# Kernel tuning notes

Hardware: AMD Instinct MI355X
Metric: run time of the kernel (lower is better)

## Reference

```python
import jax, jax.numpy as jnp
import numpy as np

N_EMBD = 768
N_HEAD = 12
NEG = -1e9  # finite stand-in for -inf in the causal part of the FIRE mask


def setup_inputs() -> dict:
    key = jax.random.key(0)
    ks = jax.random.split(key, 6)
    B, T, C = 4, 2048, N_EMBD
    x = jax.random.normal(ks[0], (B, T, C), jnp.float32)
    # FIRE-style per-head additive relative-position bias, masked causally
    bias = jax.random.normal(ks[1], (1, N_HEAD, T, T), jnp.float32)
    causal = jnp.tril(jnp.ones((T, T), bool))
    fire_causal_mask = jnp.where(causal, bias, NEG)
    W_attn = jax.random.normal(ks[2], (C, 3 * C), jnp.float32) * (1.0 / np.sqrt(C))
    b_attn = jax.random.normal(ks[3], (3 * C,), jnp.float32) * 0.02
    W_proj = jax.random.normal(ks[4], (C, C), jnp.float32) * (1.0 / np.sqrt(C))
    b_proj = jax.random.normal(ks[5], (C,), jnp.float32) * 0.02
    return {"x": x, "fire_causal_mask": fire_causal_mask, "W_attn": W_attn,
            "b_attn": b_attn, "W_proj": W_proj, "b_proj": b_proj}


def reference(x, fire_causal_mask, W_attn, b_attn, W_proj, b_proj):
    B, T, C = x.shape
    hd = C // N_HEAD
    qkv = x @ W_attn + b_attn                       # [B, T, 3C]
    q, k, v = jnp.split(qkv, 3, axis=-1)

    def to_heads(t):  # [B, T, C] -> [B, H, T, hd]
        return t.reshape(B, T, N_HEAD, hd).transpose(0, 2, 1, 3)

    q, k, v = to_heads(q), to_heads(k), to_heads(v)
    scale = 1.0 / np.sqrt(hd)
    # SDPA with additive float attn_mask: softmax(q k^T / sqrt(d) + mask) v
    scores = jnp.einsum('bhqd,bhkd->bhqk', q, k) * scale + fire_causal_mask
    p = jax.nn.softmax(scores, axis=-1)
    y = jnp.einsum('bhqk,bhkd->bhqd', p, v)         # [B, H, T, hd]
    y = y.transpose(0, 2, 1, 3).reshape(B, T, C)
    return y @ W_proj + b_proj
```

## Files before the change

### kernel.cpp

```cpp
#include <hip/hip_runtime.h>
#include <hip/hip_bf16.h>
#include <stdint.h>

#define N_HEADC 12
#define T_SEQ   2048
#define C_EMBD  768
#define HD      64

typedef short s16x8 __attribute__((ext_vector_type(8)));
typedef float f32x4 __attribute__((ext_vector_type(4)));
typedef unsigned short u16;
typedef unsigned int   u32;
typedef unsigned long long u64;

__device__ __forceinline__ u16 f2bf(float f) {
  u32 u = __builtin_bit_cast(u32, f);
  u32 r = (u + 0x7FFFu + ((u >> 16) & 1u)) >> 16;
  return (u16)r;
}

__device__ __forceinline__ void async16(const void* g, void* l) {
  u64 ga = (u64)g;
  u32 la = (u32)(u64)l;
  __builtin_amdgcn_global_load_lds(
      (const __attribute__((address_space(1))) u32*)ga,
      (__attribute__((address_space(3))) u32*)la, 16, 0, 0);
}


__global__ __launch_bounds__(256) void k_prep(
    const float4* __restrict__ x4, ushort4* __restrict__ xb4,
    const float* __restrict__ Wa, u16* __restrict__ wat,
    const float* __restrict__ Wp, u16* __restrict__ wpt) {
  __shared__ float tl[64 * 65];
  int bx = blockIdx.x;
  int tid = threadIdx.x;
  if (bx < 6144) {
    int i = bx * 256 + tid;
    float4 v = x4[i];
    ushort4 o;
    o.x = f2bf(v.x); o.y = f2bf(v.y); o.z = f2bf(v.z); o.w = f2bf(v.w);
    xb4[i] = o;
    return;
  }
  const float* in; u16* out; int Kdim, Ndim, n0, k0;
  if (bx < 6144 + 432) {
    int idx = bx - 6144;
    in = Wa; out = wat; Kdim = C_EMBD; Ndim = 3 * C_EMBD;
    n0 = (idx % 36) * 64; k0 = (idx / 36) * 64;
  } else {
    int idx = bx - 6576;
    in = Wp; out = wpt; Kdim = C_EMBD; Ndim = C_EMBD;
    n0 = (idx % 12) * 64; k0 = (idx / 12) * 64;
  }
  int r0 = tid >> 4;
  int cb = (tid & 15) * 4;
#pragma unroll
  for (int g = 0; g < 4; ++g) {
    int r = r0 + g * 16;
    float4 v = *(const float4*)&in[(size_t)(k0 + r) * Ndim + n0 + cb];
    tl[r * 65 + cb + 0] = v.x;
    tl[r * 65 + cb + 1] = v.y;
    tl[r * 65 + cb + 2] = v.z;
    tl[r * 65 + cb + 3] = v.w;
  }
  __syncthreads();
  int rr0 = tid >> 3;
  int cc = (tid & 7) * 8;
#pragma unroll
  for (int g = 0; g < 2; ++g) {
    int rr = rr0 + g * 32;
    u16 tmp[8];
#pragma unroll
    for (int j = 0; j < 8; ++j) tmp[j] = f2bf(tl[(cc + j) * 65 + rr]);
    *(uint4*)&out[(size_t)(n0 + rr) * Kdim + k0 + cc] = *(uint4*)tmp;
  }
}

__global__ __launch_bounds__(256) void k_transpose_v(const u16* __restrict__ v,
                                                     u16* __restrict__ vt) {
  __shared__ u16 tl[64 * 65];
  int t0 = blockIdx.x * 64;
  int bh = blockIdx.y;
  int tid = threadIdx.x;
  const u16* vb = v + (size_t)bh * T_SEQ * HD;
  u16* vtb = vt + (size_t)bh * HD * T_SEQ;
#pragma unroll
  for (int g = 0; g < 2; ++g) {
    int id = g * 256 + tid;
    int r = id >> 3, c = id & 7;
    uint4 raw = *(const uint4*)&vb[(size_t)(t0 + r) * HD + c * 8];
    u16 tmp[8];
    *(uint4*)tmp = raw;
#pragma unroll
    for (int j = 0; j < 8; ++j) tl[r * 65 + c * 8 + j] = tmp[j];
  }
  __syncthreads();
#pragma unroll
  for (int g = 0; g < 2; ++g) {
    int id = g * 256 + tid;
    int d = id >> 3, cw = id & 7;
    u16 tmp[8];
#pragma unroll
    for (int j = 0; j < 8; ++j) tmp[j] = tl[(cw * 8 + j) * 65 + d];
    *(uint4*)&vtb[(size_t)d * T_SEQ + t0 + cw * 8] = *(uint4*)tmp;
  }
}


#define GEMM_BODY(K)                                                          \
  __shared__ __align__(16) u16 Al[128 * 64];                                  \
  __shared__ __align__(16) u16 Bl[128 * 64];                                  \
  int n0 = blockIdx.x * 128, m0 = blockIdx.y * 128;                           \
  int tid = threadIdx.x, lane = tid & 63;                                     \
  int w = tid >> 6, quad = lane >> 4, l16 = lane & 15;                        \
  int wm = (w >> 1) * 64, wn = (w & 1) * 64;                                  \
  f32x4 acc[4][4];                                                            \
  _Pragma("unroll") for (int a = 0; a < 4; ++a)                               \
      _Pragma("unroll") for (int b = 0; b < 4; ++b)                           \
          acc[a][b] = (f32x4){0.f, 0.f, 0.f, 0.f};                            \
  for (int kt = 0; kt < (K); kt += 64) {                                      \
    __syncthreads();                                                          \
    _Pragma("unroll") for (int g = 0; g < 4; ++g) {                           \
      int id = g * 256 + tid;                                                 \
      int r = id >> 3, c = id & 7, cs = c ^ (r & 7);                          \
      async16(A + (size_t)(m0 + r) * (K) + kt + cs * 8, (char*)Al + id * 16); \
      async16(Bt + (size_t)(n0 + r) * (K) + kt + cs * 8, (char*)Bl + id * 16);\
    }                                                                         \
    __syncthreads();                                                          \
    _Pragma("unroll") for (int s = 0; s < 2; ++s) {                           \
      s16x8 af[4], bfr[4];                                                    \
      _Pragma("unroll") for (int mi = 0; mi < 4; ++mi) {                      \
        int m = wm + mi * 16 + l16;                                           \
        af[mi] = *(const s16x8*)&Al[m * 64 + (((s * 4 + quad) ^ (m & 7)) * 8)];\
      }                                                                       \
      _Pragma("unroll") for (int ni = 0; ni < 4; ++ni) {                      \
        int n = wn + ni * 16 + l16;                                           \
        bfr[ni] = *(const s16x8*)&Bl[n * 64 + (((s * 4 + quad) ^ (n & 7)) * 8)];\
      }                                                                       \
      _Pragma("unroll") for (int mi = 0; mi < 4; ++mi)                        \
          _Pragma("unroll") for (int ni = 0; ni < 4; ++ni)                    \
              acc[mi][ni] = __builtin_amdgcn_mfma_f32_16x16x32_bf16(          \
                  af[mi], bfr[ni], acc[mi][ni], 0, 0, 0);                     \
    }                                                                         \
  }

__global__ __launch_bounds__(256) void k_gemm_qkv(
    const u16* __restrict__ A, const u16* __restrict__ Bt,
    const float* __restrict__ bias, u16* __restrict__ qh,
    u16* __restrict__ kh, u16* __restrict__ vh) {
  GEMM_BODY(C_EMBD)
#pragma unroll
  for (int ni = 0; ni < 4; ++ni) {
    int n = n0 + wn + ni * 16 + l16;
    float bv = bias[n];
    int part = n / C_EMBD;
    int nn = n - part * C_EMBD;
    int hh = nn >> 6, d = nn & 63;
    u16* dst = part == 0 ? qh : (part == 1 ? kh : vh);
#pragma unroll
    for (int mi = 0; mi < 4; ++mi) {
      int mbase = m0 + wm + mi * 16 + quad * 4;
#pragma unroll
      for (int r = 0; r < 4; ++r) {
        int m = mbase + r;
        int b = m >> 11, t = m & 2047;
        dst[((size_t)(b * N_HEADC + hh) * T_SEQ + t) * HD + d] =
            f2bf(acc[mi][ni][r] + bv);
      }
    }
  }
}


__global__ __launch_bounds__(256) void k_gemm_out(
    const u16* __restrict__ A, const u16* __restrict__ Bt,
    const float* __restrict__ bias, float* __restrict__ out) {
  __shared__ __align__(16) u16 Al[128 * 64];
  __shared__ __align__(16) u16 Bl[64 * 64];
  int n0 = blockIdx.x * 64, m0 = blockIdx.y * 128;
  int tid = threadIdx.x, lane = tid & 63;
  int w = tid >> 6, quad = lane >> 4, l16 = lane & 15;
  int wm = (w >> 1) * 64, wn = (w & 1) * 32;
  f32x4 acc[4][2];
#pragma unroll
  for (int a = 0; a < 4; ++a)
#pragma unroll
    for (int b = 0; b < 2; ++b) acc[a][b] = (f32x4){0.f, 0.f, 0.f, 0.f};
  for (int kt = 0; kt < C_EMBD; kt += 64) {
    __syncthreads();
#pragma unroll
    for (int g = 0; g < 4; ++g) {
      int id = g * 256 + tid;
      int r = id >> 3, c = id & 7, cs = c ^ (r & 7);
      async16(A + (size_t)(m0 + r) * C_EMBD + kt + cs * 8, (char*)Al + id * 16);
    }
#pragma unroll
    for (int g = 0; g < 2; ++g) {
      int id = g * 256 + tid;
      int r = id >> 3, c = id & 7, cs = c ^ (r & 7);
      async16(Bt + (size_t)(n0 + r) * C_EMBD + kt + cs * 8, (char*)Bl + id * 16);
    }
    __syncthreads();
#pragma unroll
    for (int s = 0; s < 2; ++s) {
      s16x8 af[4], bfr[2];
#pragma unroll
      for (int mi = 0; mi < 4; ++mi) {
        int m = wm + mi * 16 + l16;
        af[mi] = *(const s16x8*)&Al[m * 64 + (((s * 4 + quad) ^ (m & 7)) * 8)];
      }
#pragma unroll
      for (int ni = 0; ni < 2; ++ni) {
        int n = wn + ni * 16 + l16;
        bfr[ni] = *(const s16x8*)&Bl[n * 64 + (((s * 4 + quad) ^ (n & 7)) * 8)];
      }
#pragma unroll
      for (int mi = 0; mi < 4; ++mi)
#pragma unroll
        for (int ni = 0; ni < 2; ++ni)
          acc[mi][ni] = __builtin_amdgcn_mfma_f32_16x16x32_bf16(
              af[mi], bfr[ni], acc[mi][ni], 0, 0, 0);
    }
  }
#pragma unroll
  for (int ni = 0; ni < 2; ++ni) {
    int n = n0 + wn + ni * 16 + l16;
    float bv = bias[n];
#pragma unroll
    for (int mi = 0; mi < 4; ++mi) {
      int mbase = m0 + wm + mi * 16 + quad * 4;
#pragma unroll
      for (int r = 0; r < 4; ++r)
        out[(size_t)(mbase + r) * C_EMBD + n] = acc[mi][ni][r] + bv;
    }
  }
}


__global__ __launch_bounds__(256, 4) void k_attn(
    const u16* __restrict__ qh, const u16* __restrict__ kh,
    const u16* __restrict__ vth, const float* __restrict__ mask,
    u16* __restrict__ y) {
  __shared__ __align__(16) u16 Kl[2][64 * 64];
  __shared__ __align__(16) u16 Vl[2][64 * 64];
  __shared__ __align__(16) u16 Pl[4][16 * 64];
  int bx0 = blockIdx.x;
  int by = blockIdx.y;
  int h = by >> 2, b = by & 3;
  int bh = b * N_HEADC + h;
  int tid = threadIdx.x, lane = tid & 63;
  int w = tid >> 6, quad = lane >> 4, l16 = lane & 15;

  const u16* kg = kh + (size_t)bh * T_SEQ * HD;
  const u16* vg = vth + (size_t)bh * HD * T_SEQ;

  int r_st = tid >> 3, c_st = tid & 7, cs_st = c_st ^ (r_st & 7);
  int r_st2 = r_st + 32, cs_st2 = c_st ^ (r_st2 & 7);
  int id0 = tid * 16, id1 = (256 + tid) * 16;

#pragma unroll 1
  for (int ph = 0; ph < 2; ++ph) {
    int bx = ph == 0 ? (31 - bx0) : bx0;
    int qw = bx * 64 + w * 16;

    const u16* qg = qh + ((size_t)bh * T_SEQ + qw + l16) * HD;
    s16x8 qf0 = *(const s16x8*)(qg + quad * 8);
    s16x8 qf1 = *(const s16x8*)(qg + 32 + quad * 8);
    const float* mg = mask + ((size_t)h * T_SEQ + qw + quad * 4) * T_SEQ + l16;

    f32x4 yacc[4];
#pragma unroll
    for (int i = 0; i < 4; ++i) yacc[i] = (f32x4){0.f, 0.f, 0.f, 0.f};
    float lsum[4] = {0.f, 0.f, 0.f, 0.f};

    int nkt = bx + 1;
    if (ph) __syncthreads();
    async16(kg + (size_t)r_st * HD + cs_st * 8, (char*)Kl[0] + id0);
    async16(vg + (size_t)r_st * T_SEQ + cs_st * 8, (char*)Vl[0] + id0);
    async16(kg + (size_t)r_st2 * HD + cs_st2 * 8, (char*)Kl[0] + id1);
    async16(vg + (size_t)r_st2 * T_SEQ + cs_st2 * 8, (char*)Vl[0] + id1);

    float mcur[16];
#pragma unroll
    for (int r = 0; r < 4; ++r)
#pragma unroll
      for (int nt = 0; nt < 4; ++nt)
        mcur[r * 4 + nt] = mg[(size_t)r * T_SEQ + nt * 16];

    for (int kt = 0; kt < nkt; ++kt) {
      int cur = kt & 1;
      __syncthreads();
      if (kt + 1 < nkt) {
        int nb = (kt + 1) * 64;
        async16(kg + (size_t)(nb + r_st) * HD + cs_st * 8, (char*)Kl[1 - cur] + id0);
        async16(vg + (size_t)r_st * T_SEQ + nb + cs_st * 8, (char*)Vl[1 - cur] + id0);
        async16(kg + (size_t)(nb + r_st2) * HD + cs_st2 * 8, (char*)Kl[1 - cur] + id1);
        async16(vg + (size_t)r_st2 * T_SEQ + nb + cs_st2 * 8, (char*)Vl[1 - cur] + id1);
      }
      int nb_m = (kt + 1 < nkt ? kt + 1 : kt) * 64;
      float mnxt[16];
#pragma unroll
      for (int r = 0; r < 4; ++r)
#pragma unroll
        for (int nt = 0; nt < 4; ++nt)
          mnxt[r * 4 + nt] = mg[(size_t)r * T_SEQ + nb_m + nt * 16];

      f32x4 sacc[4];
#pragma unroll
      for (int nt = 0; nt < 4; ++nt) sacc[nt] = (f32x4){0.f, 0.f, 0.f, 0.f};
#pragma unroll
      for (int nt = 0; nt < 4; ++nt) {
        int row = nt * 16 + l16;
        s16x8 kf0 = *(const s16x8*)&Kl[cur][row * 64 + ((quad ^ (row & 7)) * 8)];
        sacc[nt] = __builtin_amdgcn_mfma_f32_16x16x32_bf16(qf0, kf0, sacc[nt], 0, 0, 0);
        s16x8 kf1 = *(const s16x8*)&Kl[cur][row * 64 + (((4 + quad) ^ (row & 7)) * 8)];
        sacc[nt] = __builtin_amdgcn_mfma_f32_16x16x32_bf16(qf1, kf1, sacc[nt], 0, 0, 0);
      }

      u16* pw = &Pl[w][0];
#pragma unroll
      for (int r = 0; r < 4; ++r) {
        int prow = quad * 4 + r;
#pragma unroll
        for (int nt = 0; nt < 4; ++nt) {
          float val = __expf(fmaf(sacc[nt][r], 0.125f, mcur[r * 4 + nt]));
          lsum[r] += val;
          u32 u = __builtin_bit_cast(u32, val);
          int chunk = (nt * 2 + (l16 >> 3)) ^ (prow & 7);
          pw[prow * 64 + chunk * 8 + (l16 & 7)] = (u16)((u + 0x8000u) >> 16);
        }
      }

#pragma unroll
      for (int s = 0; s < 2; ++s) {
        s16x8 pf = *(const s16x8*)&Pl[w][l16 * 64 + (((s * 4 + quad) ^ (l16 & 7)) * 8)];
#pragma unroll
        for (int nt = 0; nt < 4; ++nt) {
          int row = nt * 16 + l16;
          s16x8 vf = *(const s16x8*)&Vl[cur][row * 64 + (((s * 4 + quad) ^ (row & 7)) * 8)];
          yacc[nt] = __builtin_amdgcn_mfma_f32_16x16x32_bf16(pf, vf, yacc[nt], 0, 0, 0);
        }
      }

#pragma unroll
      for (int i = 0; i < 16; ++i) mcur[i] = mnxt[i];
    }

    u16* yb = y + ((size_t)b * T_SEQ + qw + quad * 4) * C_EMBD + h * HD + l16;
#pragma unroll
    for (int r = 0; r < 4; ++r) {
      float l = lsum[r];
      l += __shfl_xor(l, 1);
      l += __shfl_xor(l, 2);
      l += __shfl_xor(l, 4);
      l += __shfl_xor(l, 8);
      float inv = 1.0f / l;
#pragma unroll
      for (int nt = 0; nt < 4; ++nt)
        yb[(size_t)r * C_EMBD + nt * 16] = f2bf(yacc[nt][r] * inv);
    }
  }
}


extern "C" void kernel_launch(void* const* d_in, const int* in_sizes, int n_in,
                              void* d_out, int out_size, void* d_ws, size_t ws_size,
                              hipStream_t stream) {
  (void)in_sizes; (void)n_in; (void)out_size; (void)ws_size;
  const float* x      = (const float*)d_in[0];
  const float* maskp  = (const float*)d_in[1];
  const float* W_attn = (const float*)d_in[2];
  const float* b_attn = (const float*)d_in[3];
  const float* W_proj = (const float*)d_in[4];
  const float* b_proj = (const float*)d_in[5];
  float* out = (float*)d_out;

  char* ws = (char*)d_ws;
  u16* xb  = (u16*)(ws + 0);
  u16* yb  = xb;
  u16* wat = (u16*)(ws + 12582912);
  u16* wpt = (u16*)(ws + 16121856);
  u16* qh  = (u16*)(ws + 17301504);
  u16* kh  = (u16*)(ws + 29884416);
  u16* vh  = (u16*)(ws + 42467328);
  u16* vth = (u16*)(ws + 55050240);

  k_prep<<<6720, 256, 0, stream>>>((const float4*)x, (ushort4*)xb,
                                   W_attn, wat, W_proj, wpt);
  k_gemm_qkv<<<dim3(18, 64), 256, 0, stream>>>(xb, wat, b_attn, qh, kh, vh);
  k_transpose_v<<<dim3(32, 48), 256, 0, stream>>>(vh, vth);
  k_attn<<<dim3(16, 48), 256, 0, stream>>>(qh, kh, vth, maskp, yb);
  k_gemm_out<<<dim3(12, 64), 256, 0, stream>>>(yb, wpt, b_proj, out);
}
```

Measured before the change: 415.6 us.

## Load K and V fragments directly from global memory instead of LDS staging

```diff
diff --git a/kernel.cpp b/kernel.cpp
--- a/kernel.cpp
+++ b/kernel.cpp
@@ -238,12 +238,10 @@
 }
 
 
-__global__ __launch_bounds__(256, 4) void k_attn(
+__global__ __launch_bounds__(256, 3) void k_attn(
     const u16* __restrict__ qh, const u16* __restrict__ kh,
     const u16* __restrict__ vth, const float* __restrict__ mask,
     u16* __restrict__ y) {
-  __shared__ __align__(16) u16 Kl[2][64 * 64];
-  __shared__ __align__(16) u16 Vl[2][64 * 64];
   __shared__ __align__(16) u16 Pl[4][16 * 64];
   int bx0 = blockIdx.x;
   int by = blockIdx.y;
@@ -252,12 +250,8 @@
   int tid = threadIdx.x, lane = tid & 63;
   int w = tid >> 6, quad = lane >> 4, l16 = lane & 15;
 
-  const u16* kg = kh + (size_t)bh * T_SEQ * HD;
-  const u16* vg = vth + (size_t)bh * HD * T_SEQ;
-
-  int r_st = tid >> 3, c_st = tid & 7, cs_st = c_st ^ (r_st & 7);
-  int r_st2 = r_st + 32, cs_st2 = c_st ^ (r_st2 & 7);
-  int id0 = tid * 16, id1 = (256 + tid) * 16;
+  const u16* kb = kh + ((size_t)bh * T_SEQ + l16) * HD + quad * 8;
+  const u16* vb = vth + ((size_t)bh * HD + l16) * T_SEQ + quad * 8;
 
 #pragma unroll 1
   for (int ph = 0; ph < 2; ++ph) {
@@ -275,11 +269,6 @@
     float lsum[4] = {0.f, 0.f, 0.f, 0.f};
 
     int nkt = bx + 1;
-    if (ph) __syncthreads();
-    async16(kg + (size_t)r_st * HD + cs_st * 8, (char*)Kl[0] + id0);
-    async16(vg + (size_t)r_st * T_SEQ + cs_st * 8, (char*)Vl[0] + id0);
-    async16(kg + (size_t)r_st2 * HD + cs_st2 * 8, (char*)Kl[0] + id1);
-    async16(vg + (size_t)r_st2 * T_SEQ + cs_st2 * 8, (char*)Vl[0] + id1);
 
     float mcur[16];
 #pragma unroll
@@ -289,15 +278,7 @@
         mcur[r * 4 + nt] = mg[(size_t)r * T_SEQ + nt * 16];
 
     for (int kt = 0; kt < nkt; ++kt) {
-      int cur = kt & 1;
-      __syncthreads();
-      if (kt + 1 < nkt) {
-        int nb = (kt + 1) * 64;
-        async16(kg + (size_t)(nb + r_st) * HD + cs_st * 8, (char*)Kl[1 - cur] + id0);
-        async16(vg + (size_t)r_st * T_SEQ + nb + cs_st * 8, (char*)Vl[1 - cur] + id0);
-        async16(kg + (size_t)(nb + r_st2) * HD + cs_st2 * 8, (char*)Kl[1 - cur] + id1);
-        async16(vg + (size_t)r_st2 * T_SEQ + nb + cs_st2 * 8, (char*)Vl[1 - cur] + id1);
-      }
+      int ktb = kt * 64;
       int nb_m = (kt + 1 < nkt ? kt + 1 : kt) * 64;
       float mnxt[16];
 #pragma unroll
@@ -309,12 +290,12 @@
       f32x4 sacc[4];
 #pragma unroll
       for (int nt = 0; nt < 4; ++nt) sacc[nt] = (f32x4){0.f, 0.f, 0.f, 0.f};
+      const u16* kpt = kb + (size_t)ktb * HD;
 #pragma unroll
       for (int nt = 0; nt < 4; ++nt) {
-        int row = nt * 16 + l16;
-        s16x8 kf0 = *(const s16x8*)&Kl[cur][row * 64 + ((quad ^ (row & 7)) * 8)];
+        s16x8 kf0 = *(const s16x8*)(kpt + nt * 16 * HD);
+        s16x8 kf1 = *(const s16x8*)(kpt + nt * 16 * HD + 32);
         sacc[nt] = __builtin_amdgcn_mfma_f32_16x16x32_bf16(qf0, kf0, sacc[nt], 0, 0, 0);
-        s16x8 kf1 = *(const s16x8*)&Kl[cur][row * 64 + (((4 + quad) ^ (row & 7)) * 8)];
         sacc[nt] = __builtin_amdgcn_mfma_f32_16x16x32_bf16(qf1, kf1, sacc[nt], 0, 0, 0);
       }
 
@@ -332,13 +313,13 @@
         }
       }
 
+      const u16* vpt = vb + ktb;
 #pragma unroll
       for (int s = 0; s < 2; ++s) {
         s16x8 pf = *(const s16x8*)&Pl[w][l16 * 64 + (((s * 4 + quad) ^ (l16 & 7)) * 8)];
 #pragma unroll
         for (int nt = 0; nt < 4; ++nt) {
-          int row = nt * 16 + l16;
-          s16x8 vf = *(const s16x8*)&Vl[cur][row * 64 + (((s * 4 + quad) ^ (row & 7)) * 8)];
+          s16x8 vf = *(const s16x8*)(vpt + (size_t)nt * 16 * T_SEQ + s * 32);
           yacc[nt] = __builtin_amdgcn_mfma_f32_16x16x32_bf16(pf, vf, yacc[nt], 0, 0, 0);
         }
       }
```

Result: slower. 544.2 us (+30.9%).
